# Kernel tuning notes

Hardware: AMD Instinct MI355X
Metric: run time of the kernel (lower is better)

## Reference

```python
import jax, jax.numpy as jnp
import numpy as np

TEMPERATURE = 0.07
EPS = 1e-8
B, D, C = 4096, 512, 10


def setup_inputs() -> dict:
    key = jax.random.key(0)
    k1, k2 = jax.random.split(key)
    features = jax.random.normal(k1, (B, D), dtype=jnp.float32)
    cls = jax.random.randint(k2, (B,), 0, C)
    labels = jax.nn.one_hot(cls, C, dtype=jnp.float32)  # [B, C] one-hot
    return {"features": features, "labels": labels}


def reference(features, labels):
    b = features.shape[0]
    # L2-normalize rows
    feats = features / jnp.linalg.norm(features, axis=1, keepdims=True)
    sim = jnp.clip(feats @ feats.T / TEMPERATURE, -20.0, 20.0)  # [B, B]
    eye = jnp.eye(b, dtype=bool)
    sim = jnp.where(eye, -jnp.inf, sim)  # mask self-similarity

    labels_norm = labels / (labels.sum(axis=1, keepdims=True) + EPS)
    label_sim = labels_norm @ labels_norm.T  # [B, B]
    label_sim = jnp.where(eye, 0.0, label_sim)
    pos_mask = label_sim > 0.1  # [B, B] bool

    exp_sim = jnp.exp(sim)  # diag -> exp(-inf) = 0
    pos_sum = jnp.sum(jnp.where(pos_mask, exp_sim, 0.0), axis=1)  # [B]
    all_sum = jnp.sum(exp_sim, axis=1)  # diag already zero => off-diagonal sum
    loss_i = -jnp.log(pos_sum / (all_sum + EPS) + EPS)  # [B]

    valid = jnp.any(pos_mask, axis=1)  # rows with >=1 positive
    n_valid = jnp.sum(valid.astype(jnp.float32))
    total = jnp.sum(jnp.where(valid, loss_i, 0.0))
    return jnp.where(n_valid > 0, total / n_valid, 0.0)
```

## Files before the change

kernel.cpp:

```cpp
#include <hip/hip_runtime.h>


#define B_ROWS 4096
#define D_DIM  512
#define C_CLS  10
#define NT     64
#define NTILES (NT * (NT + 1) / 2)

typedef __bf16 bf16x8 __attribute__((ext_vector_type(8)));
typedef float  f32x4  __attribute__((ext_vector_type(4)));

__device__ __forceinline__ void load_lds16(const __bf16* g, __bf16* l) {
  __builtin_amdgcn_global_load_lds(
      (const __attribute__((address_space(1))) unsigned int*)g,
      (__attribute__((address_space(3))) unsigned int*)l, 16, 0, 0);
}

__global__ __launch_bounds__(256) void prep_kernel(
    const float* __restrict__ feats, const float* __restrict__ labels,
    __bf16* __restrict__ F, int* __restrict__ cls,
    float* __restrict__ totals) {
  const int w = threadIdx.x >> 6, lane = threadIdx.x & 63;
  const int row = blockIdx.x * 4 + w;
  const float* fr = feats + (size_t)row * D_DIM;
  float4 v0 = ((const float4*)fr)[2 * lane];
  float4 v1 = ((const float4*)fr)[2 * lane + 1];
  float ss = v0.x*v0.x + v0.y*v0.y + v0.z*v0.z + v0.w*v0.w
           + v1.x*v1.x + v1.y*v1.y + v1.z*v1.z + v1.w*v1.w;
  #pragma unroll
  for (int m = 1; m < 64; m <<= 1) ss += __shfl_xor(ss, m, 64);
  float inv = 1.0f / sqrtf(ss);

  bf16x8 o;
  o[0] = (__bf16)(v0.x * inv); o[1] = (__bf16)(v0.y * inv);
  o[2] = (__bf16)(v0.z * inv); o[3] = (__bf16)(v0.w * inv);
  o[4] = (__bf16)(v1.x * inv); o[5] = (__bf16)(v1.y * inv);
  o[6] = (__bf16)(v1.z * inv); o[7] = (__bf16)(v1.w * inv);
  *(bf16x8*)(F + (size_t)row * D_DIM + 8 * lane) = o;

  float lv = (lane < C_CLS) ? labels[(size_t)row * C_CLS + lane] : 0.f;
  unsigned long long m = __ballot(lv > 0.5f);
  if (lane == 0) cls[row] = (int)(__ffsll((long long)m) - 1);
  if (blockIdx.x == 0 && threadIdx.x == 0) { totals[0] = 0.f; totals[1] = 0.f; }
}

__global__ __launch_bounds__(128) void sim_kernel(
    const __bf16* __restrict__ F, const int* __restrict__ cls,
    float* __restrict__ P_all, float* __restrict__ P_pos) {
  __shared__ __align__(16) __bf16 Abuf[64 * 64];
  __shared__ __align__(16) __bf16 Bbuf[64 * 64];
  __shared__ int clsA[64], clsB[64];
  __shared__ float g_row_all[64], g_row_pos[64];
  __shared__ float g_col_all[64], g_col_pos[64];

  int rem = blockIdx.x, bi = 0, rowlen = NT;
  while (rem >= rowlen) { rem -= rowlen; ++bi; --rowlen; }
  const int bj = bi + rem;
  const int i0 = bi * 64, j0 = bj * 64;
  const bool offdiag = (bi != bj);

  const int t = threadIdx.x;
  const int w = t >> 6;
  const int lane = t & 63;
  const int q = lane >> 4;
  const int cl = lane & 15;

  if (t < 64) clsA[t] = cls[i0 + t];
  else        clsB[t - 64] = cls[j0 + t - 64];
  if (t < 64) { g_col_all[t] = 0.f; g_col_pos[t] = 0.f; }

  f32x4 acc[2][4];
  #pragma unroll
  for (int ri = 0; ri < 2; ++ri)
    #pragma unroll
    for (int c = 0; c < 4; ++c) acc[ri][c] = (f32x4){0.f, 0.f, 0.f, 0.f};

  const int srow = lane >> 3;
  const int sg   = (lane & 7) ^ srow;

  for (int k0 = 0; k0 < D_DIM; k0 += 64) {
    __syncthreads();
    #pragma unroll
    for (int r = 0; r < 4; ++r) {
      const int rowbase = 32 * w + r * 8;
      load_lds16(F + (size_t)(i0 + rowbase + srow) * D_DIM + k0 + sg * 8,
                 &Abuf[rowbase * 64]);
      load_lds16(F + (size_t)(j0 + rowbase + srow) * D_DIM + k0 + sg * 8,
                 &Bbuf[rowbase * 64]);
    }
    __syncthreads();

    #pragma unroll
    for (int kk = 0; kk < 64; kk += 32) {
      const int g = (kk >> 3) + q;
      const int cc = g ^ (cl & 7);
      bf16x8 af[2], bfr[4];
      #pragma unroll
      for (int ri = 0; ri < 2; ++ri)
        af[ri] = *(const bf16x8*)&Abuf[(32 * w + 16 * ri + cl) * 64 + cc * 8];
      #pragma unroll
      for (int c = 0; c < 4; ++c)
        bfr[c] = *(const bf16x8*)&Bbuf[(16 * c + cl) * 64 + cc * 8];
      #pragma unroll
      for (int ri = 0; ri < 2; ++ri)
        #pragma unroll
        for (int c = 0; c < 4; ++c)
          acc[ri][c] = __builtin_amdgcn_mfma_f32_16x16x32_bf16(
              af[ri], bfr[c], acc[ri][c], 0, 0, 0);
    }
  }

  const float invT = 1.0f / 0.07f;
  float cs_all[4] = {0.f, 0.f, 0.f, 0.f};
  float cs_pos[4] = {0.f, 0.f, 0.f, 0.f};

  #pragma unroll
  for (int ri = 0; ri < 2; ++ri) {
    float sum_all[4] = {0.f, 0.f, 0.f, 0.f};
    float sum_pos[4] = {0.f, 0.f, 0.f, 0.f};
    #pragma unroll
    for (int c = 0; c < 4; ++c) {
      const int jloc = 16*c + cl;
      const int gj = j0 + jloc;
      const int cj = clsB[jloc];
      #pragma unroll
      for (int r = 0; r < 4; ++r) {
        const int iloc = 32*w + 16*ri + q*4 + r;
        const int gi = i0 + iloc;
        float s = acc[ri][c][r] * invT;
        s = fminf(fmaxf(s, -20.f), 20.f);
        const bool diag = (gi == gj);
        float e = diag ? 0.f : __expf(s);
        sum_all[r] += e;
        cs_all[c] += e;
        if (!diag && cj == clsA[iloc]) { sum_pos[r] += e; cs_pos[c] += e; }
      }
    }
    #pragma unroll
    for (int r = 0; r < 4; ++r) {
      float sa = sum_all[r], sp = sum_pos[r];
      #pragma unroll
      for (int m = 1; m < 16; m <<= 1) {
        sa += __shfl_xor(sa, m, 64);
        sp += __shfl_xor(sp, m, 64);
      }
      if (cl == 0) {
        const int rloc = 32*w + 16*ri + q*4 + r;
        g_row_all[rloc] = sa;
        g_row_pos[rloc] = sp;
      }
    }
  }

  if (offdiag) {
    #pragma unroll
    for (int c = 0; c < 4; ++c) {
      float sa = cs_all[c], sp = cs_pos[c];
      sa += __shfl_xor(sa, 16, 64); sa += __shfl_xor(sa, 32, 64);
      sp += __shfl_xor(sp, 16, 64); sp += __shfl_xor(sp, 32, 64);
      if (q == 0) {
        atomicAdd(&g_col_all[16*c + cl], sa);
        atomicAdd(&g_col_pos[16*c + cl], sp);
      }
    }
  }
  __syncthreads();

  if (w == 0) {
    const size_t base_row = ((size_t)bi * 64 + bj) * 64;
    P_all[base_row + lane] = g_row_all[lane];
    P_pos[base_row + lane] = g_row_pos[lane];
  } else if (offdiag) {
    const size_t base_col = ((size_t)bj * 64 + bi) * 64;
    P_all[base_col + lane] = g_col_all[lane];
    P_pos[base_col + lane] = g_col_pos[lane];
  }
}

__global__ __launch_bounds__(256) void finalize_kernel(
    const float* __restrict__ P_all, const float* __restrict__ P_pos,
    float* __restrict__ totals) {
  __shared__ float Sall[4096], Spos[4096];
  const int s = blockIdx.x;
  const int t = threadIdx.x;
  for (int i = t; i < 4096; i += 256) {
    Sall[i] = P_all[(size_t)s * 4096 + i];
    Spos[i] = P_pos[(size_t)s * 4096 + i];
  }
  __syncthreads();
  if (t < 64) {
    float a = 0.f, p = 0.f;
    #pragma unroll 8
    for (int k = 0; k < 64; ++k) {
      a += Sall[k * 64 + t];
      p += Spos[k * 64 + t];
    }
    float loss = 0.f, cnt = 0.f;
    if (p > 0.f) {
      loss = -logf(p / (a + 1e-8f) + 1e-8f);
      cnt = 1.f;
    }
    #pragma unroll
    for (int m = 1; m < 64; m <<= 1) {
      loss += __shfl_xor(loss, m, 64);
      cnt  += __shfl_xor(cnt, m, 64);
    }
    if (t == 0) {
      atomicAdd(&totals[0], loss);
      atomicAdd(&totals[1], cnt);
    }
  }
}

__global__ void div_kernel(const float* __restrict__ totals,
                           float* __restrict__ out) {
  out[0] = (totals[1] > 0.f) ? (totals[0] / totals[1]) : 0.f;
}

extern "C" void kernel_launch(void* const* d_in, const int* in_sizes, int n_in,
                              void* d_out, int out_size, void* d_ws, size_t ws_size,
                              hipStream_t stream) {
  const float* features = (const float*)d_in[0];
  const float* labels   = (const float*)d_in[1];
  float* out = (float*)d_out;

  __bf16* F      = (__bf16*)d_ws;
  int*    cls    = (int*)((char*)d_ws + (size_t)B_ROWS * D_DIM * 2);
  float*  P_all  = (float*)((char*)cls + B_ROWS * sizeof(int));
  float*  P_pos  = P_all + (size_t)NT * NT * 64;
  float*  totals = P_pos + (size_t)NT * NT * 64;

  prep_kernel<<<B_ROWS / 4, 256, 0, stream>>>(features, labels, F, cls, totals);
  sim_kernel<<<NTILES, 128, 0, stream>>>(F, cls, P_all, P_pos);
  finalize_kernel<<<NT, 256, 0, stream>>>(P_all, P_pos, totals);
  div_kernel<<<1, 1, 0, stream>>>(totals, out);
}
```

Baseline: 92.15 us.

## Load MFMA operands directly from global memory instead of staging through LDS

```diff
diff --git a/kernel.cpp b/kernel.cpp
--- a/kernel.cpp
+++ b/kernel.cpp
@@ -9,12 +9,6 @@
 
 typedef __bf16 bf16x8 __attribute__((ext_vector_type(8)));
 typedef float  f32x4  __attribute__((ext_vector_type(4)));
-
-__device__ __forceinline__ void load_lds16(const __bf16* g, __bf16* l) {
-  __builtin_amdgcn_global_load_lds(
-      (const __attribute__((address_space(1))) unsigned int*)g,
-      (__attribute__((address_space(3))) unsigned int*)l, 16, 0, 0);
-}
 
 __global__ __launch_bounds__(256) void prep_kernel(
     const float* __restrict__ feats, const float* __restrict__ labels,
@@ -47,8 +41,6 @@
 __global__ __launch_bounds__(128) void sim_kernel(
     const __bf16* __restrict__ F, const int* __restrict__ cls,
     float* __restrict__ P_all, float* __restrict__ P_pos) {
-  __shared__ __align__(16) __bf16 Abuf[64 * 64];
-  __shared__ __align__(16) __bf16 Bbuf[64 * 64];
   __shared__ int clsA[64], clsB[64];
   __shared__ float g_row_all[64], g_row_pos[64];
   __shared__ float g_col_all[64], g_col_pos[64];
@@ -65,9 +57,8 @@
   const int q = lane >> 4;
   const int cl = lane & 15;
 
-  if (t < 64) clsA[t] = cls[i0 + t];
+  if (t < 64) { clsA[t] = cls[i0 + t]; g_col_all[t] = 0.f; g_col_pos[t] = 0.f; }
   else        clsB[t - 64] = cls[j0 + t - 64];
-  if (t < 64) { g_col_all[t] = 0.f; g_col_pos[t] = 0.f; }
 
   f32x4 acc[2][4];
   #pragma unroll
@@ -75,40 +66,31 @@
     #pragma unroll
     for (int c = 0; c < 4; ++c) acc[ri][c] = (f32x4){0.f, 0.f, 0.f, 0.f};
 
-  const int srow = lane >> 3;
-  const int sg   = (lane & 7) ^ srow;
-
-  for (int k0 = 0; k0 < D_DIM; k0 += 64) {
-    __syncthreads();
-    #pragma unroll
-    for (int r = 0; r < 4; ++r) {
-      const int rowbase = 32 * w + r * 8;
-      load_lds16(F + (size_t)(i0 + rowbase + srow) * D_DIM + k0 + sg * 8,
-                 &Abuf[rowbase * 64]);
-      load_lds16(F + (size_t)(j0 + rowbase + srow) * D_DIM + k0 + sg * 8,
-                 &Bbuf[rowbase * 64]);
-    }
-    __syncthreads();
-
-    #pragma unroll
-    for (int kk = 0; kk < 64; kk += 32) {
-      const int g = (kk >> 3) + q;
-      const int cc = g ^ (cl & 7);
-      bf16x8 af[2], bfr[4];
-      #pragma unroll
-      for (int ri = 0; ri < 2; ++ri)
-        af[ri] = *(const bf16x8*)&Abuf[(32 * w + 16 * ri + cl) * 64 + cc * 8];
+  const __bf16* pa[2];
+  const __bf16* pb[4];
+  #pragma unroll
+  for (int ri = 0; ri < 2; ++ri)
+    pa[ri] = F + (size_t)(i0 + 32 * w + 16 * ri + cl) * D_DIM + q * 8;
+  #pragma unroll
+  for (int c = 0; c < 4; ++c)
+    pb[c] = F + (size_t)(j0 + 16 * c + cl) * D_DIM + q * 8;
+
+  #pragma unroll 4
+  for (int k0 = 0; k0 < D_DIM; k0 += 32) {
+    bf16x8 af[2], bfr[4];
+    #pragma unroll
+    for (int ri = 0; ri < 2; ++ri) af[ri] = *(const bf16x8*)(pa[ri] + k0);
+    #pragma unroll
+    for (int c = 0; c < 4; ++c)    bfr[c] = *(const bf16x8*)(pb[c] + k0);
+    #pragma unroll
+    for (int ri = 0; ri < 2; ++ri)
       #pragma unroll
       for (int c = 0; c < 4; ++c)
-        bfr[c] = *(const bf16x8*)&Bbuf[(16 * c + cl) * 64 + cc * 8];
-      #pragma unroll
-      for (int ri = 0; ri < 2; ++ri)
-        #pragma unroll
-        for (int c = 0; c < 4; ++c)
-          acc[ri][c] = __builtin_amdgcn_mfma_f32_16x16x32_bf16(
-              af[ri], bfr[c], acc[ri][c], 0, 0, 0);
-    }
-  }
+        acc[ri][c] = __builtin_amdgcn_mfma_f32_16x16x32_bf16(
+            af[ri], bfr[c], acc[ri][c], 0, 0, 0);
+  }
+
+  __syncthreads();
 
   const float invT = 1.0f / 0.07f;
   float cs_all[4] = {0.f, 0.f, 0.f, 0.f};
```

Measured after the change: 120.3 us. 1.31x slower.
